# Performance work log

Measured on AMD Instinct MI355X. Metric: run time of the kernel, lower is better.

## Reference

```python
import jax, jax.numpy as jnp
import numpy as np

EMBED = 1024
HEADS = 16
HEAD_DIM = EMBED // HEADS


def _rope(t):
    # t: (B, S, H, D) -> rotary embedding applied over last dim (GPT-NeoX rotate-half)
    B, S, H, D = t.shape
    half = D // 2
    inv_freq = 1.0 / (10000.0 ** (jnp.arange(0, half, dtype=jnp.float32) / half))
    freqs = jnp.arange(S, dtype=jnp.float32)[:, None] * inv_freq[None, :]  # (S, half)
    cos = jnp.cos(freqs)[None, :, None, :]
    sin = jnp.sin(freqs)[None, :, None, :]
    t1, t2 = t[..., :half], t[..., half:]
    return jnp.concatenate([t1 * cos - t2 * sin, t2 * cos + t1 * sin], axis=-1)


def setup_inputs() -> dict:
    key = jax.random.key(0)
    k1, k2, k3 = jax.random.split(key, 3)
    B, S = 2, 2048
    x = jax.random.normal(k1, (B, S, EMBED), dtype=jnp.float32)
    attn_mask = jnp.ones((B, S), dtype=bool)
    w_qkv = jax.random.normal(k2, (EMBED, 3 * EMBED), dtype=jnp.float32) * (1.0 / np.sqrt(EMBED))
    w_out = jax.random.normal(k3, (EMBED, EMBED), dtype=jnp.float32) * (1.0 / np.sqrt(EMBED))
    return {"x": x, "attn_mask": attn_mask, "w_qkv": w_qkv, "w_out": w_out, "is_causal": 1}


def reference(x, attn_mask, w_qkv, w_out, is_causal):
    B, S, E = x.shape
    qkv = x @ w_qkv                                   # (B, S, 3E)
    q, k, v = jnp.split(qkv, 3, axis=-1)
    q = q.reshape(B, S, HEADS, HEAD_DIM)
    k = k.reshape(B, S, HEADS, HEAD_DIM)
    v = v.reshape(B, S, HEADS, HEAD_DIM)
    q = _rope(q)
    k = _rope(k)
    scale = 1.0 / np.sqrt(HEAD_DIM)
    scores = jnp.einsum('bqhd,bkhd->bhqk', q, k) * scale  # (B, H, S, S)
    neg = jnp.asarray(-1e30, dtype=scores.dtype)
    if is_causal:
        causal = jnp.tril(jnp.ones((S, S), dtype=bool))
        scores = jnp.where(causal[None, None], scores, neg)
    else:
        scores = jnp.where(attn_mask[:, None, None, :], scores, neg)
    attn = jax.nn.softmax(scores, axis=-1)
    y = jnp.einsum('bhqk,bkhd->bqhd', attn, v).reshape(B, S, E)
    return y @ w_out
```

## Files before the change

kernel.cpp:

```cpp
#include <hip/hip_runtime.h>
#include <hip/hip_bf16.h>
#include <stdint.h>

typedef float v4f __attribute__((ext_vector_type(4)));
typedef short v8s __attribute__((ext_vector_type(8)));

#define LOG2E 1.44269504088896f
#define QSCALE (0.125f * LOG2E)
#define SOFTMAX_OFF 16.0f

__device__ __forceinline__ unsigned short f2bf(float f) {
    unsigned int u = __float_as_uint(f);
    u += 0x7fffu + ((u >> 16) & 1u);
    return (unsigned short)(u >> 16);
}
__device__ __forceinline__ float bf2f(unsigned short u) {
    return __uint_as_float((unsigned int)u << 16);
}

#define LDS_FENCE() __builtin_amdgcn_fence(__ATOMIC_ACQ_REL, "workgroup")

__device__ __forceinline__ void gload_lds16(const unsigned short* g, unsigned short* s) {
    __builtin_amdgcn_global_load_lds(
        (const __attribute__((address_space(1))) unsigned int*)g,
        (__attribute__((address_space(3))) unsigned int*)s, 16, 0, 0);
}

__global__ void k_cast_bf16(const float* __restrict__ src,
                            unsigned short* __restrict__ dst, int n4) {
    int i = blockIdx.x * blockDim.x + threadIdx.x;
    int stride = gridDim.x * blockDim.x;
    for (; i < n4; i += stride) {
        float4 v = ((const float4*)src)[i];
        ushort4 o;
        o.x = f2bf(v.x); o.y = f2bf(v.y); o.z = f2bf(v.z); o.w = f2bf(v.w);
        ((ushort4*)dst)[i] = o;
    }
}

__global__ void k_transpose_cast(const float* __restrict__ src,
                                 unsigned short* __restrict__ dst, int K, int N) {
    __shared__ unsigned short tile[64][65];
    int kb = blockIdx.y * 64, nb = blockIdx.x * 64;
    int t = threadIdx.x;
    for (int i = 0; i < 16; ++i) {
        int e = t + i * 256;
        int n_l = e & 63, k_l = e >> 6;
        tile[n_l][k_l] = f2bf(src[(size_t)(kb + k_l) * N + nb + n_l]);
    }
    __syncthreads();
    for (int i = 0; i < 16; ++i) {
        int e = t + i * 256;
        int k_l = e & 63, n_l = e >> 6;
        dst[(size_t)(nb + n_l) * K + kb + k_l] = tile[n_l][k_l];
    }
}

template<bool BF16OUT>
__global__ __launch_bounds__(256) void k_gemm_bt(
    const unsigned short* __restrict__ A,
    const unsigned short* __restrict__ Bt,
    void* __restrict__ Cv, int M, int N, int K) {
    __shared__ __align__(16) unsigned short Ab[128 * 32];
    __shared__ __align__(16) unsigned short Bb[128 * 32];
    const int t = threadIdx.x;
    const int w = t >> 6, l = t & 63, quad = l >> 4, ln = l & 15;
    const int wm = (w >> 1) * 64, wn = (w & 1) * 64;
    const int mb = blockIdx.y * 128, nb = blockIdx.x * 128;

    v4f acc[4][4];
#pragma unroll
    for (int i = 0; i < 4; ++i)
#pragma unroll
        for (int j = 0; j < 4; ++j) acc[i][j] = (v4f){0.f, 0.f, 0.f, 0.f};

    for (int k0 = 0; k0 < K; k0 += 32) {
        __syncthreads();
#pragma unroll
        for (int u = 0; u < 2; ++u) {
            int e = t + u * 256;
            gload_lds16(A + (size_t)(mb + (e >> 2)) * K + k0 + (e & 3) * 8,
                        &Ab[(size_t)(w * 64 + u * 256) * 8]);
            gload_lds16(Bt + (size_t)(nb + (e >> 2)) * K + k0 + (e & 3) * 8,
                        &Bb[(size_t)(w * 64 + u * 256) * 8]);
        }
        __syncthreads();
        v8s af[4], bfr[4];
#pragma unroll
        for (int i = 0; i < 4; ++i)
            af[i] = *(const v8s*)&Ab[(wm + i * 16 + ln) * 32 + quad * 8];
#pragma unroll
        for (int j = 0; j < 4; ++j)
            bfr[j] = *(const v8s*)&Bb[(wn + j * 16 + ln) * 32 + quad * 8];
#pragma unroll
        for (int i = 0; i < 4; ++i)
#pragma unroll
            for (int j = 0; j < 4; ++j)
                acc[i][j] = __builtin_amdgcn_mfma_f32_16x16x32_bf16(
                    af[i], bfr[j], acc[i][j], 0, 0, 0);
    }

#pragma unroll
    for (int i = 0; i < 4; ++i) {
        int r0 = mb + wm + i * 16 + quad * 4;
#pragma unroll
        for (int j = 0; j < 4; ++j) {
            int c0 = nb + wn + j * 16 + ln;
#pragma unroll
            for (int r = 0; r < 4; ++r) {
                if (BF16OUT)
                    ((unsigned short*)Cv)[(size_t)(r0 + r) * N + c0] = f2bf(acc[i][j][r]);
                else
                    ((float*)Cv)[(size_t)(r0 + r) * N + c0] = acc[i][j][r];
            }
        }
    }
}

__global__ void k_rope_split(const unsigned short* __restrict__ qkvb,
                             unsigned short* __restrict__ Qg,
                             unsigned short* __restrict__ Kg,
                             unsigned short* __restrict__ Vt) {
    __shared__ unsigned short vtile[64][65];
    const int bh = blockIdx.y, sb = blockIdx.x * 64;
    const int b = bh >> 4, h = bh & 15;
    const int t = threadIdx.x;

    for (int i = 0; i < 8; ++i) {
        int e = t + i * 256;
        int d = e & 31, s_l = e >> 5;
        int s = sb + s_l;
        const unsigned short* row = qkvb + (size_t)(b * 2048 + s) * 3072 + h * 64;
        float inv = __expf(-(float)d * 0.28782313662425572f);
        float ang = (float)s * inv;
        float sn, cs;
        sincosf(ang, &sn, &cs);
        float q1 = bf2f(row[d]), q2 = bf2f(row[d + 32]);
        float k1 = bf2f(row[1024 + d]), k2 = bf2f(row[1024 + d + 32]);
        size_t qb = (size_t)(bh * 2048 + s) * 64;
        Qg[qb + d]      = f2bf((q1 * cs - q2 * sn) * QSCALE);
        Qg[qb + d + 32] = f2bf((q2 * cs + q1 * sn) * QSCALE);
        Kg[qb + d]      = f2bf(k1 * cs - k2 * sn);
        Kg[qb + d + 32] = f2bf(k2 * cs + k1 * sn);
    }
    for (int i = 0; i < 16; ++i) {
        int e = t + i * 256;
        int d = e & 63, s_l = e >> 6;
        vtile[d][s_l] = qkvb[(size_t)(b * 2048 + sb + s_l) * 3072 + 2048 + h * 64 + d];
    }
    __syncthreads();
    for (int i = 0; i < 16; ++i) {
        int e = t + i * 256;
        int s_l = e & 63, d = e >> 6;
        Vt[(size_t)(bh * 64 + d) * 2048 + sb + s_l] = vtile[d][s_l];
    }
}

__global__ __launch_bounds__(256) void k_flash(
    const unsigned short* __restrict__ Qg,
    const unsigned short* __restrict__ Kg,
    const unsigned short* __restrict__ Vt,
    unsigned short* __restrict__ Og) {
    __shared__ __align__(16) unsigned short Kb[2][64 * 64];
    __shared__ __align__(16) unsigned short Vb[2][64 * 64];
    __shared__ __align__(16) unsigned short P[4][16][72];

    const int id = blockIdx.x;
    const int xcd = id & 7, slot = id >> 3;
    const int bh = xcd * 4 + (slot & 3);
    const int qt = 31 - (slot >> 2);
    const int qbase = qt * 64;
    const int nit = qt + 1;

    const int t = threadIdx.x, w = t >> 6, l = t & 63, quad = l >> 4, ln = l & 15;
    const int b = bh >> 4, h = bh & 15;

    const unsigned short* Qp = Qg + (size_t)bh * 2048 * 64;
    const unsigned short* Kp = Kg + (size_t)bh * 2048 * 64;
    const unsigned short* Vp = Vt + (size_t)bh * 64 * 2048;

    unsigned kst[2], vst[2];
    int cchunk = l & 7, rloc = l >> 3;
#pragma unroll
    for (int j = 0; j < 2; ++j) {
        int c = w + j * 4;
        int rr = c * 8 + rloc;
        int g = (cchunk + rr) & 7;
        kst[j] = (unsigned)(rr * 64 + g * 8);
        vst[j] = (unsigned)(rr * 2048 + g * 8);
    }
    const int c0 = ((quad - ln) & 7) * 8;
    const int c1 = ((quad + 4 - ln) & 7) * 8;
    const v8s ones = {0x3F80, 0x3F80, 0x3F80, 0x3F80, 0x3F80, 0x3F80, 0x3F80, 0x3F80};

    const int qrow = qbase + w * 16 + ln;
    v8s qf0 = *(const v8s*)(Qp + (size_t)qrow * 64 + quad * 8);
    v8s qf1 = *(const v8s*)(Qp + (size_t)qrow * 64 + quad * 8 + 32);

    v4f oacc[5];
#pragma unroll
    for (int dt = 0; dt < 5; ++dt) oacc[dt] = (v4f){0.f, 0.f, 0.f, 0.f};

    auto stage = [&](int buf, int kvb) {
        const unsigned short* kg = Kp + (size_t)kvb * 64;
        const unsigned short* vg = Vp + kvb;
#pragma unroll
        for (int j = 0; j < 2; ++j) {
            int c = w + j * 4;
            gload_lds16(kg + kst[j], &Kb[buf][c * 512]);
            gload_lds16(vg + vst[j], &Vb[buf][c * 512]);
        }
    };

    auto compute = [&](int buf, int it) {
        v4f sc[4];
#pragma unroll
        for (int kt = 0; kt < 4; ++kt) {
            int row = kt * 16 + ln;
            v8s k0 = *(const v8s*)&Kb[buf][row * 64 + c0];
            v8s k1 = *(const v8s*)&Kb[buf][row * 64 + c1];
            sc[kt] = (v4f){0.f, 0.f, 0.f, 0.f};
            sc[kt] = __builtin_amdgcn_mfma_f32_16x16x32_bf16(qf0, k0, sc[kt], 0, 0, 0);
            sc[kt] = __builtin_amdgcn_mfma_f32_16x16x32_bf16(qf1, k1, sc[kt], 0, 0, 0);
        }
        if (it == qt) {
            int q0 = qbase + w * 16 + quad * 4;
#pragma unroll
            for (int kt = 0; kt < 4; ++kt) {
                int kv = qbase + kt * 16 + ln;
#pragma unroll
                for (int r = 0; r < 4; ++r)
                    if (kv > q0 + r) sc[kt][r] = -1e30f;
            }
        }
#pragma unroll
        for (int kt = 0; kt < 4; ++kt)
#pragma unroll
            for (int r = 0; r < 4; ++r)
                sc[kt][r] = exp2f(sc[kt][r] - SOFTMAX_OFF);

#pragma unroll
        for (int kt = 0; kt < 4; ++kt) {
            union { __hip_bfloat162 hh; unsigned int u; } p01, p23;
            p01.hh = __float22bfloat162_rn(make_float2(sc[kt][0], sc[kt][1]));
            p23.hh = __float22bfloat162_rn(make_float2(sc[kt][2], sc[kt][3]));
            P[w][quad * 4 + 0][kt * 16 + ln] = (unsigned short)p01.u;
            P[w][quad * 4 + 1][kt * 16 + ln] = (unsigned short)(p01.u >> 16);
            P[w][quad * 4 + 2][kt * 16 + ln] = (unsigned short)p23.u;
            P[w][quad * 4 + 3][kt * 16 + ln] = (unsigned short)(p23.u >> 16);
        }
        LDS_FENCE();
        v8s pf0 = *(const v8s*)&P[w][ln][quad * 8];
        v8s pf1 = *(const v8s*)&P[w][ln][quad * 8 + 32];
        LDS_FENCE();
#pragma unroll
        for (int dt = 0; dt < 4; ++dt) {
            int row = dt * 16 + ln;
            v8s v0 = *(const v8s*)&Vb[buf][row * 64 + c0];
            v8s v1 = *(const v8s*)&Vb[buf][row * 64 + c1];
            oacc[dt] = __builtin_amdgcn_mfma_f32_16x16x32_bf16(pf0, v0, oacc[dt], 0, 0, 0);
            oacc[dt] = __builtin_amdgcn_mfma_f32_16x16x32_bf16(pf1, v1, oacc[dt], 0, 0, 0);
        }
        oacc[4] = __builtin_amdgcn_mfma_f32_16x16x32_bf16(pf0, ones, oacc[4], 0, 0, 0);
        oacc[4] = __builtin_amdgcn_mfma_f32_16x16x32_bf16(pf1, ones, oacc[4], 0, 0, 0);
    };

    stage(0, 0);
    int it = 0;
    for (;;) {
        __syncthreads();
        stage(1, (it + 1) * 64);
        compute(0, it);
        if (++it >= nit) break;
        __syncthreads();
        stage(0, (it + 1) * 64);
        compute(1, it);
        if (++it >= nit) break;
    }

    float rden[4];
#pragma unroll
    for (int r = 0; r < 4; ++r) rden[r] = 1.f / oacc[4][r];
#pragma unroll
    for (int dt = 0; dt < 4; ++dt)
#pragma unroll
        for (int r = 0; r < 4; ++r) {
            int s = qbase + w * 16 + quad * 4 + r;
            Og[(size_t)(b * 2048 + s) * 1024 + h * 64 + dt * 16 + ln] =
                f2bf(oacc[dt][r] * rden[r]);
        }
}

extern "C" void kernel_launch(void* const* d_in, const int* in_sizes, int n_in,
                              void* d_out, int out_size, void* d_ws, size_t ws_size,
                              hipStream_t stream) {
    const float* x     = (const float*)d_in[0];
    const float* w_qkv = (const float*)d_in[2];
    const float* w_out = (const float*)d_in[3];
    char* ws = (char*)d_ws;

    unsigned short* xb    = (unsigned short*)(ws);
    unsigned short* wqkvT = (unsigned short*)(ws + (size_t)(8 << 20));
    unsigned short* woutT = (unsigned short*)(ws + (size_t)(14 << 20));
    unsigned short* qkvb  = (unsigned short*)(ws + (size_t)(16 << 20));
    unsigned short* Qg    = (unsigned short*)(ws + (size_t)(40 << 20));
    unsigned short* Kg    = (unsigned short*)(ws + (size_t)(48 << 20));
    unsigned short* Vt    = (unsigned short*)(ws + (size_t)(56 << 20));
    unsigned short* Og    = (unsigned short*)(ws + (size_t)(64 << 20));

    k_cast_bf16<<<1024, 256, 0, stream>>>(x, xb, 4096 * 1024 / 4);
    k_transpose_cast<<<dim3(48, 16), 256, 0, stream>>>(w_qkv, wqkvT, 1024, 3072);
    k_transpose_cast<<<dim3(16, 16), 256, 0, stream>>>(w_out, woutT, 1024, 1024);
    k_gemm_bt<true><<<dim3(24, 32), 256, 0, stream>>>(xb, wqkvT, qkvb, 4096, 3072, 1024);
    k_rope_split<<<dim3(32, 32), 256, 0, stream>>>(qkvb, Qg, Kg, Vt);
    k_flash<<<1024, 256, 0, stream>>>(Qg, Kg, Vt, Og);
    k_gemm_bt<false><<<dim3(8, 32), 256, 0, stream>>>(Og, woutT, (float*)d_out, 4096, 1024, 1024);
}
```

Measured before the change: 205.2 us.

## Fuse RoPE and head split into QKV GEMM epilogue, merge weight transposes

Applies rotary embedding and Q scaling directly in the QKV GEMM epilogue and writes Q, K, V in per-head layout, removing the intermediate qkv buffer round trip and the separate rope kernel. V still goes through a smaller transpose kernel. The two weight transpose launches are merged into one grid. The epilogue now computes sincos per output element with scattered 2-byte stores, which adds transcendental work and uncoalesced writes inside the GEMM.

```diff
diff --git a/kernel.cpp b/kernel.cpp
--- a/kernel.cpp
+++ b/kernel.cpp
@@ -13,9 +13,6 @@
     unsigned int u = __float_as_uint(f);
     u += 0x7fffu + ((u >> 16) & 1u);
     return (unsigned short)(u >> 16);
-}
-__device__ __forceinline__ float bf2f(unsigned short u) {
-    return __uint_as_float((unsigned int)u << 16);
 }
 
 #define LDS_FENCE() __builtin_amdgcn_fence(__ATOMIC_ACQ_REL, "workgroup")
@@ -38,10 +35,16 @@
     }
 }
 
-__global__ void k_transpose_cast(const float* __restrict__ src,
-                                 unsigned short* __restrict__ dst, int K, int N) {
+__global__ void k_transpose_both(const float* __restrict__ w_qkv,
+                                 const float* __restrict__ w_out,
+                                 unsigned short* __restrict__ wqkvT,
+                                 unsigned short* __restrict__ woutT) {
     __shared__ unsigned short tile[64][65];
-    int kb = blockIdx.y * 64, nb = blockIdx.x * 64;
+    int id = blockIdx.x;
+    const float* src; unsigned short* dst; int N, kb, nb;
+    if (id < 768) { src = w_qkv; dst = wqkvT; N = 3072; nb = (id % 48) * 64; kb = (id / 48) * 64; }
+    else { id -= 768; src = w_out; dst = woutT; N = 1024; nb = (id % 16) * 64; kb = (id / 16) * 64; }
+    const int K = 1024;
     int t = threadIdx.x;
     for (int i = 0; i < 16; ++i) {
         int e = t + i * 256;
@@ -53,6 +56,110 @@
         int e = t + i * 256;
         int k_l = e & 63, n_l = e >> 6;
         dst[(size_t)(nb + n_l) * K + kb + k_l] = tile[n_l][k_l];
+    }
+}
+
+__global__ __launch_bounds__(256) void k_gemm_qkv(
+    const unsigned short* __restrict__ A,
+    const unsigned short* __restrict__ Bt,
+    unsigned short* __restrict__ Qg,
+    unsigned short* __restrict__ Kg,
+    unsigned short* __restrict__ Vg) {
+    const int K = 1024, N = 3072;
+    __shared__ __align__(16) unsigned short Ab[128 * 32];
+    __shared__ __align__(16) unsigned short Bb[128 * 32];
+    const int t = threadIdx.x;
+    const int w = t >> 6, l = t & 63, quad = l >> 4, ln = l & 15;
+    const int wm = (w >> 1) * 64, wn = (w & 1) * 64;
+    const int mb = blockIdx.y * 128, nb = blockIdx.x * 128;
+
+    v4f acc[4][4];
+#pragma unroll
+    for (int i = 0; i < 4; ++i)
+#pragma unroll
+        for (int j = 0; j < 4; ++j) acc[i][j] = (v4f){0.f, 0.f, 0.f, 0.f};
+
+    for (int k0 = 0; k0 < K; k0 += 32) {
+        __syncthreads();
+#pragma unroll
+        for (int u = 0; u < 2; ++u) {
+            int e = t + u * 256;
+            gload_lds16(A + (size_t)(mb + (e >> 2)) * K + k0 + (e & 3) * 8,
+                        &Ab[(size_t)(w * 64 + u * 256) * 8]);
+            gload_lds16(Bt + (size_t)(nb + (e >> 2)) * K + k0 + (e & 3) * 8,
+                        &Bb[(size_t)(w * 64 + u * 256) * 8]);
+        }
+        __syncthreads();
+        v8s af[4], bfr[4];
+#pragma unroll
+        for (int i = 0; i < 4; ++i)
+            af[i] = *(const v8s*)&Ab[(wm + i * 16 + ln) * 32 + quad * 8];
+#pragma unroll
+        for (int j = 0; j < 4; ++j)
+            bfr[j] = *(const v8s*)&Bb[(wn + j * 16 + ln) * 32 + quad * 8];
+#pragma unroll
+        for (int i = 0; i < 4; ++i)
+#pragma unroll
+            for (int j = 0; j < 4; ++j)
+                acc[i][j] = __builtin_amdgcn_mfma_f32_16x16x32_bf16(
+                    af[i], bfr[j], acc[i][j], 0, 0, 0);
+    }
+
+    const int col0 = nb + wn;
+    const int region = col0 >> 10;
+    const int h = (col0 & 1023) >> 6;
+    unsigned short* dst = (region == 0) ? Qg : (region == 1) ? Kg : Vg;
+
+    if (region == 2) {
+#pragma unroll
+        for (int i = 0; i < 4; ++i)
+#pragma unroll
+            for (int r = 0; r < 4; ++r) {
+                int row = mb + wm + i * 16 + quad * 4 + r;
+                int s = row & 2047, b = row >> 11;
+                size_t base = ((size_t)(b * 16 + h) * 2048 + s) * 64;
+#pragma unroll
+                for (int j = 0; j < 4; ++j)
+                    dst[base + j * 16 + ln] = f2bf(acc[i][j][r]);
+            }
+    } else {
+        const float scale = (region == 0) ? QSCALE : 1.0f;
+#pragma unroll
+        for (int jj = 0; jj < 2; ++jj) {
+            float inv = __expf(-(float)(jj * 16 + ln) * 0.28782313662425572f);
+#pragma unroll
+            for (int i = 0; i < 4; ++i)
+#pragma unroll
+                for (int r = 0; r < 4; ++r) {
+                    int row = mb + wm + i * 16 + quad * 4 + r;
+                    int s = row & 2047, b = row >> 11;
+                    float sn, cs;
+                    sincosf((float)s * inv, &sn, &cs);
+                    float t1 = acc[i][jj][r], t2 = acc[i][jj + 2][r];
+                    size_t base = ((size_t)(b * 16 + h) * 2048 + s) * 64;
+                    dst[base + jj * 16 + ln]      = f2bf((t1 * cs - t2 * sn) * scale);
+                    dst[base + jj * 16 + ln + 32] = f2bf((t2 * cs + t1 * sn) * scale);
+                }
+        }
+    }
+}
+
+__global__ void k_vtrans(const unsigned short* __restrict__ Vg,
+                         unsigned short* __restrict__ Vt) {
+    __shared__ unsigned short vtile[64][65];
+    const int bh = blockIdx.y, sb = blockIdx.x * 64;
+    const int t = threadIdx.x;
+    const unsigned short* src = Vg + (size_t)bh * 2048 * 64;
+    for (int i = 0; i < 16; ++i) {
+        int e = t + i * 256;
+        int d = e & 63, s_l = e >> 6;
+        vtile[d][s_l] = src[(size_t)(sb + s_l) * 64 + d];
+    }
+    __syncthreads();
+    for (int i = 0; i < 16; ++i) {
+        int e = t + i * 256;
+        int s_l = e & 63, d = e >> 6;
+        Vt[(size_t)(bh * 64 + d) * 2048 + sb + s_l] = vtile[d][s_l];
     }
 }
 
@@ -117,45 +224,6 @@
     }
 }
 
-__global__ void k_rope_split(const unsigned short* __restrict__ qkvb,
-                             unsigned short* __restrict__ Qg,
-                             unsigned short* __restrict__ Kg,
-                             unsigned short* __restrict__ Vt) {
-    __shared__ unsigned short vtile[64][65];
-    const int bh = blockIdx.y, sb = blockIdx.x * 64;
-    const int b = bh >> 4, h = bh & 15;
-    const int t = threadIdx.x;
-
-    for (int i = 0; i < 8; ++i) {
-        int e = t + i * 256;
-        int d = e & 31, s_l = e >> 5;
-        int s = sb + s_l;
-        const unsigned short* row = qkvb + (size_t)(b * 2048 + s) * 3072 + h * 64;
-        float inv = __expf(-(float)d * 0.28782313662425572f);
-        float ang = (float)s * inv;
-        float sn, cs;
-        sincosf(ang, &sn, &cs);
-        float q1 = bf2f(row[d]), q2 = bf2f(row[d + 32]);
-        float k1 = bf2f(row[1024 + d]), k2 = bf2f(row[1024 + d + 32]);
-        size_t qb = (size_t)(bh * 2048 + s) * 64;
-        Qg[qb + d]      = f2bf((q1 * cs - q2 * sn) * QSCALE);
-        Qg[qb + d + 32] = f2bf((q2 * cs + q1 * sn) * QSCALE);
-        Kg[qb + d]      = f2bf(k1 * cs - k2 * sn);
-        Kg[qb + d + 32] = f2bf(k2 * cs + k1 * sn);
-    }
-    for (int i = 0; i < 16; ++i) {
-        int e = t + i * 256;
-        int d = e & 63, s_l = e >> 6;
-        vtile[d][s_l] = qkvb[(size_t)(b * 2048 + sb + s_l) * 3072 + 2048 + h * 64 + d];
-    }
-    __syncthreads();
-    for (int i = 0; i < 16; ++i) {
-        int e = t + i * 256;
-        int s_l = e & 63, d = e >> 6;
-        Vt[(size_t)(bh * 64 + d) * 2048 + sb + s_l] = vtile[d][s_l];
-    }
-}
-
 __global__ __launch_bounds__(256) void k_flash(
     const unsigned short* __restrict__ Qg,
     const unsigned short* __restrict__ Kg,
@@ -302,17 +370,16 @@
     unsigned short* xb    = (unsigned short*)(ws);
     unsigned short* wqkvT = (unsigned short*)(ws + (size_t)(8 << 20));
     unsigned short* woutT = (unsigned short*)(ws + (size_t)(14 << 20));
-    unsigned short* qkvb  = (unsigned short*)(ws + (size_t)(16 << 20));
-    unsigned short* Qg    = (unsigned short*)(ws + (size_t)(40 << 20));
-    unsigned short* Kg    = (unsigned short*)(ws + (size_t)(48 << 20));
-    unsigned short* Vt    = (unsigned short*)(ws + (size_t)(56 << 20));
-    unsigned short* Og    = (unsigned short*)(ws + (size_t)(64 << 20));
+    unsigned short* Qg    = (unsigned short*)(ws + (size_t)(16 << 20));
+    unsigned short* Kg    = (unsigned short*)(ws + (size_t)(24 << 20));
+    unsigned short* Vg    = (unsigned short*)(ws + (size_t)(32 << 20));
+    unsigned short* Vt    = (unsigned short*)(ws + (size_t)(40 << 20));
+    unsigned short* Og    = (unsigned short*)(ws + (size_t)(48 << 20));
 
     k_cast_bf16<<<1024, 256, 0, stream>>>(x, xb, 4096 * 1024 / 4);
-    k_transpose_cast<<<dim3(48, 16), 256, 0, stream>>>(w_qkv, wqkvT, 1024, 3072);
-    k_transpose_cast<<<dim3(16, 16), 256, 0, stream>>>(w_out, woutT, 1024, 1024);
-    k_gemm_bt<true><<<dim3(24, 32), 256, 0, stream>>>(xb, wqkvT, qkvb, 4096, 3072, 1024);
-    k_rope_split<<<dim3(32, 32), 256, 0, stream>>>(qkvb, Qg, Kg, Vt);
+    k_transpose_both<<<1024, 256, 0, stream>>>(w_qkv, w_out, wqkvT, woutT);
+    k_gemm_qkv<<<dim3(24, 32), 256, 0, stream>>>(xb, wqkvT, Qg, Kg, Vg);
+    k_vtrans<<<dim3(32, 32), 256, 0, stream>>>(Vg, Vt);
     k_flash<<<1024, 256, 0, stream>>>(Qg, Kg, Vt, Og);
     k_gemm_bt<false><<<dim3(8, 32), 256, 0, stream>>>(Og, woutT, (float*)d_out, 4096, 1024, 1024);
 }
```

After: 214.3 us. 4.5% more time.
